# Performance work log

Measured on AMD Instinct MI355X. Metric: run time of the kernel, lower is better.

Reference implementation:

```python
import jax, jax.numpy as jnp
import numpy as np

N = 131072          # total sampled proposals (flattened over batch)
D = 1024            # num_extractor_out
C = 21              # num_classes (VOC: 20 + background)


def setup_inputs() -> dict:
    key = jax.random.key(0)
    k1, k2, k3 = jax.random.split(key, 3)
    features = jax.random.normal(k1, (N, D), dtype=jnp.float32)
    # Linear weights stored as [in, out] so y = x @ W + b
    W_cls = jax.random.normal(k2, (D, C), dtype=jnp.float32) * (1.0 / np.sqrt(D))
    b_cls = jnp.zeros((C,), dtype=jnp.float32)
    W_tf = jax.random.normal(k3, (D, C * 4), dtype=jnp.float32) * (1.0 / np.sqrt(D))
    b_tf = jnp.zeros((C * 4,), dtype=jnp.float32)
    return {"features": features, "W_cls": W_cls, "b_cls": b_cls, "W_tf": W_tf, "b_tf": b_tf}


def reference(features, W_cls, b_cls, W_tf, b_tf):
    # ROI.forward with identity extractor / no pre/post transforms.
    proposal_classes = features @ W_cls + b_cls                    # [N, C]
    proposal_transformers = features @ W_tf + b_tf                 # [N, C*4]
    proposal_transformers = proposal_transformers.reshape(features.shape[0], C, 4)
    return proposal_classes, proposal_transformers
```

## Files before the change

kernel.cpp:

```cpp
#include <hip/hip_runtime.h>
#include <hip/hip_bf16.h>

#define NROWS 131072
#define DK    1024
#define CCLS  21
#define CTF   84
#define NCOL  105
#define NCT   7
#define BM    16
#define SLABF 256
#define NSLAB (DK / SLABF)
#define ROWB  1040

typedef __attribute__((ext_vector_type(4))) float f32x4;
typedef __attribute__((ext_vector_type(8))) short bf16x8;

typedef const __attribute__((address_space(1))) void GV;
typedef __attribute__((address_space(3))) void LV;

__device__ __forceinline__ unsigned short f2bf_rne(float x) {
    union { float f; unsigned u; } v; v.f = x;
    unsigned r = v.u + 0x7fffu + ((v.u >> 16) & 1u);
    return (unsigned short)(r >> 16);
}

__device__ __forceinline__ unsigned pack2(float lo, float hi) {
    union { float f; unsigned u; } a, b; a.f = lo; b.f = hi;
    return ((a.u + 0x8000u) >> 16) | ((b.u + 0x8000u) & 0xffff0000u);
}

__device__ __forceinline__ bf16x8 cvt8v(const f32x4 lo, const f32x4 hi) {
    union { unsigned u[4]; bf16x8 v; } r;
    r.u[0] = pack2(lo[0], lo[1]);
    r.u[1] = pack2(lo[2], lo[3]);
    r.u[2] = pack2(hi[0], hi[1]);
    r.u[3] = pack2(hi[2], hi[3]);
    return r.v;
}

__global__ void pack_B_kernel(const float* __restrict__ Wc,
                              const float* __restrict__ Wt,
                              unsigned short* __restrict__ Bp) {
    const int frag = blockIdx.x;
    const int kt = frag / NCT, ct = frag % NCT;
    const int lane = threadIdx.x;
    const int col = ct * 16 + (lane & 15);
    const int k0  = kt * 32 + ((lane >> 4) << 3);
    bf16x8 o;
#pragma unroll
    for (int j = 0; j < 8; ++j) {
        const int k = k0 + j;
        float v = 0.0f;
        if (col < CCLS)      v = Wc[k * CCLS + col];
        else if (col < NCOL) v = Wt[k * CTF + (col - CCLS)];
        o[j] = (short)f2bf_rne(v);
    }
    *reinterpret_cast<bf16x8*>(Bp + ((size_t)frag * 64 + lane) * 8) = o;
}

__global__ __launch_bounds__(256, 4)
void roi_gemm_kernel(const float* __restrict__ F,
                     const unsigned short* __restrict__ Bp,
                     const float* __restrict__ bcls,
                     const float* __restrict__ btf,
                     float* __restrict__ out) {
    __shared__ __align__(16) unsigned char smem[2 * BM * ROWB];

    const int t    = threadIdx.x;
    const int wave = t >> 6;
    const int lane = t & 63;
    const int fr   = lane & 15;
    const int fq   = lane >> 4;
    const long rw  = (long)blockIdx.x * BM;

    const int rcol0 = (t >> 2) & 15;
    float biasr[NCT];
#pragma unroll
    for (int ct = 0; ct < NCT; ++ct) {
        const int col = ct * 16 + rcol0;
        biasr[ct] = (col < CCLS) ? bcls[col]
                  : (col < NCOL) ? btf[col - CCLS] : 0.0f;
    }

    const unsigned short* bb = Bp + (size_t)lane * 8;

    f32x4 acc[NCT];
#pragma unroll
    for (int ct = 0; ct < NCT; ++ct) acc[ct] = (f32x4){0.f, 0.f, 0.f, 0.f};

#define STAGE(BUF, S) do {                                                    \
    _Pragma("unroll")                                                         \
    for (int q = 0; q < 4; ++q) {                                             \
        const int row = wave * 4 + q;                                         \
        __builtin_amdgcn_global_load_lds(                                     \
            (GV*)(F + ((size_t)(rw + row)) * DK + (size_t)(S) * SLABF         \
                  + lane * 4),                                                \
            (LV*)(smem + (BUF) * BM * ROWB + row * ROWB), 16, 0, 0);          \
    }                                                                         \
} while (0)

    STAGE(0, 0);

    for (int s = 0; s < NSLAB; ++s) {
        const int buf = s & 1;

        if (s + 1 < NSLAB) {
            STAGE(buf ^ 1, s + 1);
            __builtin_amdgcn_sched_barrier(0);
            asm volatile("s_waitcnt vmcnt(4)" ::: "memory");
        } else {
            asm volatile("s_waitcnt vmcnt(0)" ::: "memory");
        }
        __builtin_amdgcn_sched_barrier(0);
        __builtin_amdgcn_s_barrier();
        __builtin_amdgcn_sched_barrier(0);

        const unsigned char* bufb = smem + buf * BM * ROWB;
#pragma unroll
        for (int jj = 0; jj < 2; ++jj) {
            const int ktg = s * 8 + wave * 2 + jj;
            bf16x8 bfr[NCT];
#pragma unroll
            for (int ct = 0; ct < NCT; ++ct)
                bfr[ct] = *reinterpret_cast<const bf16x8*>(
                    bb + ((size_t)(ktg * NCT + ct) * 512));
            const unsigned char* ap =
                bufb + fr * ROWB + (wave * 2 + jj) * 128 + fq * 32;
            const f32x4 lo = *reinterpret_cast<const f32x4*>(ap);
            const f32x4 hi = *reinterpret_cast<const f32x4*>(ap + 16);
            const bf16x8 a = cvt8v(lo, hi);
#pragma unroll
            for (int ct = 0; ct < NCT; ++ct)
                acc[ct] = __builtin_amdgcn_mfma_f32_16x16x32_bf16(
                    a, bfr[ct], acc[ct], 0, 0, 0);
        }

        __builtin_amdgcn_sched_barrier(0);
        __builtin_amdgcn_s_barrier();
        __builtin_amdgcn_sched_barrier(0);
    }
#undef STAGE

    float* sf = reinterpret_cast<float*>(smem);
#pragma unroll
    for (int ct = 0; ct < NCT; ++ct)
        *reinterpret_cast<f32x4*>(sf + ((wave * NCT + ct) << 8) + (lane << 2)) =
            acc[ct];
    __syncthreads();

    float* out_tf = out + (size_t)NROWS * CCLS;
    const long grow = rw + ((t >> 6) << 2) + (t & 3);
#pragma unroll
    for (int ct = 0; ct < NCT; ++ct) {
        const int col = ct * 16 + rcol0;
        if (col >= NCOL) continue;
        const float v = sf[(0 * NCT + ct) * 256 + t] +
                        sf[(1 * NCT + ct) * 256 + t] +
                        sf[(2 * NCT + ct) * 256 + t] +
                        sf[(3 * NCT + ct) * 256 + t] + biasr[ct];
        if (col < CCLS) out[grow * CCLS + col] = v;
        else            out_tf[grow * CTF + (col - CCLS)] = v;
    }
}

extern "C" void kernel_launch(void* const* d_in, const int* in_sizes, int n_in,
                              void* d_out, int out_size, void* d_ws, size_t ws_size,
                              hipStream_t stream) {
    const float* F  = (const float*)d_in[0];
    const float* Wc = (const float*)d_in[1];
    const float* bc = (const float*)d_in[2];
    const float* Wt = (const float*)d_in[3];
    const float* bt = (const float*)d_in[4];
    unsigned short* Bp = (unsigned short*)d_ws;

    pack_B_kernel<<<NCT * (DK / 32), 64, 0, stream>>>(Wc, Wt, Bp);
    roi_gemm_kernel<<<NROWS / BM, 256, 0, stream>>>(F, Bp, bc, bt,
                                                    (float*)d_out);
}
```

Measured before the change: 154.5 us.

## Convert A to bf16 before LDS store with swizzled layout and register prefetch

Replaces the direct global-to-LDS fp32 staging with register loads of the next slab that are converted to bf16 and written into a swizzled, half-size LDS buffer after the MFMAs of the current slab. The A fragment is then read as a single 16-byte bf16 load per MFMA group, with no conversion in the inner loop. B fragments for both k-steps are hoisted ahead, and bias loads move to the epilogue. The aim is to cut LDS traffic and bank conflicts and to overlap global loads with compute, at the cost of more VGPRs and a full barrier each slab.

```diff
diff --git a/kernel.cpp b/kernel.cpp
--- a/kernel.cpp
+++ b/kernel.cpp
@@ -10,13 +10,10 @@
 #define BM    16
 #define SLABF 256
 #define NSLAB (DK / SLABF)
-#define ROWB  1040
 
 typedef __attribute__((ext_vector_type(4))) float f32x4;
 typedef __attribute__((ext_vector_type(8))) short bf16x8;
-
-typedef const __attribute__((address_space(1))) void GV;
-typedef __attribute__((address_space(3))) void LV;
+typedef __attribute__((ext_vector_type(2))) unsigned int u32x2;
 
 __device__ __forceinline__ unsigned short f2bf_rne(float x) {
     union { float f; unsigned u; } v; v.f = x;
@@ -27,15 +24,6 @@
 __device__ __forceinline__ unsigned pack2(float lo, float hi) {
     union { float f; unsigned u; } a, b; a.f = lo; b.f = hi;
     return ((a.u + 0x8000u) >> 16) | ((b.u + 0x8000u) & 0xffff0000u);
-}
-
-__device__ __forceinline__ bf16x8 cvt8v(const f32x4 lo, const f32x4 hi) {
-    union { unsigned u[4]; bf16x8 v; } r;
-    r.u[0] = pack2(lo[0], lo[1]);
-    r.u[1] = pack2(lo[2], lo[3]);
-    r.u[2] = pack2(hi[0], hi[1]);
-    r.u[3] = pack2(hi[2], hi[3]);
-    return r.v;
 }
 
 __global__ void pack_B_kernel(const float* __restrict__ Wc,
@@ -64,7 +52,7 @@
                      const float* __restrict__ bcls,
                      const float* __restrict__ btf,
                      float* __restrict__ out) {
-    __shared__ __align__(16) unsigned char smem[2 * BM * ROWB];
+    __shared__ __align__(16) unsigned char smem[28672];
 
     const int t    = threadIdx.x;
     const int wave = t >> 6;
@@ -73,73 +61,80 @@
     const int fq   = lane >> 4;
     const long rw  = (long)blockIdx.x * BM;
 
-    const int rcol0 = (t >> 2) & 15;
-    float biasr[NCT];
-#pragma unroll
-    for (int ct = 0; ct < NCT; ++ct) {
-        const int col = ct * 16 + rcol0;
-        biasr[ct] = (col < CCLS) ? bcls[col]
-                  : (col < NCOL) ? btf[col - CCLS] : 0.0f;
-    }
-
     const unsigned short* bb = Bp + (size_t)lane * 8;
+    const float* abase = F + (size_t)(rw + wave * 4) * DK + lane * 4;
 
     f32x4 acc[NCT];
 #pragma unroll
     for (int ct = 0; ct < NCT; ++ct) acc[ct] = (f32x4){0.f, 0.f, 0.f, 0.f};
 
-#define STAGE(BUF, S) do {                                                    \
-    _Pragma("unroll")                                                         \
-    for (int q = 0; q < 4; ++q) {                                             \
-        const int row = wave * 4 + q;                                         \
-        __builtin_amdgcn_global_load_lds(                                     \
-            (GV*)(F + ((size_t)(rw + row)) * DK + (size_t)(S) * SLABF         \
-                  + lane * 4),                                                \
-            (LV*)(smem + (BUF) * BM * ROWB + row * ROWB), 16, 0, 0);          \
-    }                                                                         \
-} while (0)
+#define AWADDR(BUF, Q) (smem + (BUF) * 8192 + (wave * 4 + (Q)) * 512 +        \
+    (((lane >> 1) ^ ((wave * 4 + (Q)) & 7)) << 4) + ((lane & 1) << 3))
 
-    STAGE(0, 0);
+    {
+        f32x4 v0[4];
+#pragma unroll
+        for (int q = 0; q < 4; ++q)
+            v0[q] = *reinterpret_cast<const f32x4*>(abase + (size_t)q * DK);
+#pragma unroll
+        for (int q = 0; q < 4; ++q) {
+            u32x2 d;
+            d[0] = pack2(v0[q][0], v0[q][1]);
+            d[1] = pack2(v0[q][2], v0[q][3]);
+            *reinterpret_cast<u32x2*>(AWADDR(0, q)) = d;
+        }
+    }
+    __syncthreads();
 
+#pragma unroll
     for (int s = 0; s < NSLAB; ++s) {
         const int buf = s & 1;
 
-        if (s + 1 < NSLAB) {
-            STAGE(buf ^ 1, s + 1);
-            __builtin_amdgcn_sched_barrier(0);
-            asm volatile("s_waitcnt vmcnt(4)" ::: "memory");
-        } else {
-            asm volatile("s_waitcnt vmcnt(0)" ::: "memory");
-        }
-        __builtin_amdgcn_sched_barrier(0);
-        __builtin_amdgcn_s_barrier();
-        __builtin_amdgcn_sched_barrier(0);
-
-        const unsigned char* bufb = smem + buf * BM * ROWB;
+        bf16x8 bfr[2][NCT];
 #pragma unroll
         for (int jj = 0; jj < 2; ++jj) {
             const int ktg = s * 8 + wave * 2 + jj;
-            bf16x8 bfr[NCT];
 #pragma unroll
             for (int ct = 0; ct < NCT; ++ct)
-                bfr[ct] = *reinterpret_cast<const bf16x8*>(
+                bfr[jj][ct] = *reinterpret_cast<const bf16x8*>(
                     bb + ((size_t)(ktg * NCT + ct) * 512));
-            const unsigned char* ap =
-                bufb + fr * ROWB + (wave * 2 + jj) * 128 + fq * 32;
-            const f32x4 lo = *reinterpret_cast<const f32x4*>(ap);
-            const f32x4 hi = *reinterpret_cast<const f32x4*>(ap + 16);
-            const bf16x8 a = cvt8v(lo, hi);
+        }
+        __builtin_amdgcn_sched_barrier(0);
+
+        f32x4 v[4];
+        if (s + 1 < NSLAB) {
+#pragma unroll
+            for (int q = 0; q < 4; ++q)
+                v[q] = *reinterpret_cast<const f32x4*>(
+                    abase + (size_t)q * DK + (s + 1) * SLABF);
+        }
+        __builtin_amdgcn_sched_barrier(0);
+
+#pragma unroll
+        for (int jj = 0; jj < 2; ++jj) {
+            const int lt = wave * 2 + jj;
+            const bf16x8 a = *reinterpret_cast<const bf16x8*>(
+                smem + buf * 8192 + fr * 512 +
+                ((((lt << 2) | fq) ^ (fr & 7)) << 4));
 #pragma unroll
             for (int ct = 0; ct < NCT; ++ct)
                 acc[ct] = __builtin_amdgcn_mfma_f32_16x16x32_bf16(
-                    a, bfr[ct], acc[ct], 0, 0, 0);
+                    a, bfr[jj][ct], acc[ct], 0, 0, 0);
         }
+        __builtin_amdgcn_sched_barrier(0);
 
-        __builtin_amdgcn_sched_barrier(0);
-        __builtin_amdgcn_s_barrier();
-        __builtin_amdgcn_sched_barrier(0);
+        if (s + 1 < NSLAB) {
+#pragma unroll
+            for (int q = 0; q < 4; ++q) {
+                u32x2 d;
+                d[0] = pack2(v[q][0], v[q][1]);
+                d[1] = pack2(v[q][2], v[q][3]);
+                *reinterpret_cast<u32x2*>(AWADDR(buf ^ 1, q)) = d;
+            }
+        }
+        __syncthreads();
     }
-#undef STAGE
+#undef AWADDR
 
     float* sf = reinterpret_cast<float*>(smem);
 #pragma unroll
@@ -148,6 +143,7 @@
             acc[ct];
     __syncthreads();
 
+    const int rcol0 = (t >> 2) & 15;
     float* out_tf = out + (size_t)NROWS * CCLS;
     const long grow = rw + ((t >> 6) << 2) + (t & 3);
 #pragma unroll
@@ -157,7 +153,8 @@
         const float v = sf[(0 * NCT + ct) * 256 + t] +
                         sf[(1 * NCT + ct) * 256 + t] +
                         sf[(2 * NCT + ct) * 256 + t] +
-                        sf[(3 * NCT + ct) * 256 + t] + biasr[ct];
+                        sf[(3 * NCT + ct) * 256 + t] +
+                        ((col < CCLS) ? bcls[col] : btf[col - CCLS]);
         if (col < CCLS) out[grow * CCLS + col] = v;
         else            out_tf[grow * CTF + (col - CCLS)] = v;
     }
```

Result: faster. 145.1 us, median of 3 (-6.0%).
